# Optimization experiments

Measured on AMD Instinct MI355X. Metric: run time of the kernel, lower is better.

## Reference

```python
import jax, jax.numpy as jnp
import numpy as np

N, E, IN_FEATS, D, H, DIST_DIM, NBOUND = 10000, 160000, 128, 64, 4, 32, 31

def setup_inputs() -> dict:
    key = jax.random.key(0)
    ks = jax.random.split(key, 16)
    gain = 5.0 / 3.0  # tanh gain
    def xavier(k, shape):
        # xavier_normal over the last two dims (fan_in, fan_out) as torch does per-slice
        fan_in, fan_out = shape[-2], shape[-1]
        std = gain * np.sqrt(2.0 / (fan_in + fan_out))
        return jax.random.normal(k, shape, dtype=jnp.float32) * std
    inp = {
        'feat': jax.random.normal(ks[0], (N, IN_FEATS), dtype=jnp.float32),
        'locations': jax.random.normal(ks[1], (N, 3), dtype=jnp.float32),
        'src': jax.random.randint(ks[2], (E,), 0, N),
        'dst': jax.random.randint(ks[3], (E,), 0, N),
        'inter_ids': jax.random.randint(ks[4], (E, H), 0, N),
        'W_fc': xavier(ks[5], (IN_FEATS, H * D)),
        'embed_table': jax.random.normal(ks[6], (NBOUND + 1, DIST_DIM), dtype=jnp.float32),
        'G': xavier(ks[7], (H, DIST_DIM, D)),
        'attn_fc1': xavier(ks[8], (H, 2 * D, D)),
        'attn_fc2': xavier(ks[9], (H, 2 * D, D)),
        'attn_fc3': xavier(ks[10], (H, 2 * D, D)),
        'attn_fc': xavier(ks[11], (H, 3 * D, D)),
        'attn_out': xavier(ks[12], (H, D, 1)),
        'boundaries': jnp.linspace(0.1, 3.1, NBOUND).astype(jnp.float32),
    }
    return inp


def reference(feat, locations, W_fc, embed_table, G, attn_fc1, attn_fc2, attn_fc3,
              attn_fc, attn_out, boundaries, src, dst, inter_ids):
    n = feat.shape[0]
    h = (feat @ W_fc).reshape(n, H, D)                      # [N,H,D]
    pos = locations                                          # [N,3]
    src_pos = pos[src]                                       # [E,3]
    dst_pos = pos[dst]                                       # [E,3]
    inter_pos = pos[inter_ids]                               # [E,H,3]
    h_src = h[src]                                           # [E,H,D]
    h_dst = h[dst]                                           # [E,H,D]
    head_idx = jnp.arange(H)[None, :]
    inter_h = h[inter_ids, head_idx, :]                      # [E,H,D] per-head gather

    e_count = src.shape[0]
    dist1 = jnp.broadcast_to(jnp.linalg.norm(dst_pos - src_pos, axis=-1)[:, None], (e_count, H))
    dist2 = jnp.linalg.norm(dst_pos[:, None, :] - inter_pos, axis=-1)   # [E,H]
    dist_ = jnp.linalg.norm(src_pos[:, None, :] - inter_pos, axis=-1)   # [E,H]

    def dist_embed(dist):
        idx = jnp.searchsorted(boundaries, dist, side='left')  # torch.bucketize(right=False)
        e = embed_table[idx]                                   # [E,H,DIST_DIM]
        return jnp.einsum('ehk,hkd->ehd', e, G)                # [E,H,D]

    de1 = dist_embed(dist1)
    de2 = dist_embed(dist2)
    de_ = dist_embed(dist_)

    d1 = jnp.einsum('ehk,hkd->ehd', jnp.concatenate([h_src, de1], axis=-1), attn_fc1)
    d2 = jnp.einsum('ehk,hkd->ehd', jnp.concatenate([inter_h, de2], axis=-1), attn_fc2)
    d3 = jnp.einsum('ehk,hkd->ehd', jnp.concatenate([h_dst, de_], axis=-1), attn_fc3)

    h_c = jnp.tanh(jnp.einsum('ehk,hkd->ehd', jnp.concatenate([d1, d2, d3], axis=-1), attn_fc))
    e_score = jnp.einsum('ehd,hdo->eho', h_c, attn_out)[..., 0]        # [E,H]

    # edge softmax grouped by destination node
    m = jax.ops.segment_max(e_score, dst, num_segments=n)              # [N,H]
    ex = jnp.exp(e_score - m[dst])
    den = jax.ops.segment_sum(ex, dst, num_segments=n)                 # [N,H]
    a = ex / den[dst]                                                  # [E,H]

    ft = jax.ops.segment_sum(a[:, :, None] * h_src, dst, num_segments=n)  # [N,H,D]
    rst = jnp.mean(ft, axis=1)                                          # merge='mean' -> [N,D]
    return rst
```

## Files before the change

kernel.cpp:

```cpp
#include <hip/hip_runtime.h>
#include <hip/hip_fp16.h>
#include <math.h>

#define N_NODES 10000
#define E_EDGES 160000
#define DMODEL 64
#define H 4
#define NBOUND 31
#define SLOTS 64
#define QREC 1024

typedef _Float16 half8 __attribute__((ext_vector_type(8)));
typedef float floatx4 __attribute__((ext_vector_type(4)));

__device__ __forceinline__ void mm4(const float* __restrict__ S, int aoff,
                                    int astride, int boff, int i0, int j,
                                    int Kdim, float o[4]) {
  float a0 = 0.f, a1 = 0.f, a2 = 0.f, a3 = 0.f;
  for (int t4 = 0; t4 < (Kdim >> 2); ++t4) {
    float4 f0 = *(const float4*)&S[aoff + (i0 + 0) * astride + t4 * 4];
    float4 f1 = *(const float4*)&S[aoff + (i0 + 1) * astride + t4 * 4];
    float4 f2 = *(const float4*)&S[aoff + (i0 + 2) * astride + t4 * 4];
    float4 f3 = *(const float4*)&S[aoff + (i0 + 3) * astride + t4 * 4];
    float b0 = S[boff + (t4 * 4 + 0) * 64 + j];
    float b1 = S[boff + (t4 * 4 + 1) * 64 + j];
    float b2 = S[boff + (t4 * 4 + 2) * 64 + j];
    float b3 = S[boff + (t4 * 4 + 3) * 64 + j];
    a0 += f0.x * b0 + f0.y * b1 + f0.z * b2 + f0.w * b3;
    a1 += f1.x * b0 + f1.y * b1 + f1.z * b2 + f1.w * b3;
    a2 += f2.x * b0 + f2.y * b1 + f2.z * b2 + f2.w * b3;
    a3 += f3.x * b0 + f3.y * b1 + f3.z * b2 + f3.w * b3;
  }
  o[0] = a0; o[1] = a1; o[2] = a2; o[3] = a3;
}

__device__ __forceinline__ int didx(const float* __restrict__ bnd2, float d) {
  int g = (int)(d * 10.0f);
  g = (g < 0) ? 0 : ((g > 31) ? 31 : g);
  g += (bnd2[g + 1] < d) ? 1 : 0;
  g -= (bnd2[g] >= d) ? 1 : 0;
  return g;
}

__global__ __launch_bounds__(512) void prep_kernel(
    const float* __restrict__ fc1, const float* __restrict__ fc2,
    const float* __restrict__ fc3, const float* __restrict__ fcc,
    const float* __restrict__ Wfc, const float* __restrict__ pos,
    __half* __restrict__ bigWT, int* __restrict__ cnt,
    float4* __restrict__ pos4) {
  __shared__ __align__(16) float S[12288];
  int bi = blockIdx.x;
  int tid = threadIdx.x;
  if (bi >= 24) {
    int n = (bi - 24) * 512 + tid;
    if (n < N_NODES) {
      cnt[n] = 0;
      pos4[n] = make_float4(pos[n * 3], pos[n * 3 + 1], pos[n * 3 + 2], 0.f);
    }
    return;
  }
  int ca = bi / 12;
  int kh = bi % 12;
  int k = kh >> 2, h = kh & 3;
  const float* fck = (k == 0) ? fc1 : (k == 1) ? fc2 : fc3;
  fck += h * 128 * 64;
  const float* F = fcc + h * 192 * 64 + k * 64 * 64;
  int j = tid & 63, ig = tid >> 6;
  float o[4];
  #pragma unroll
  for (int u = 0; u < 2; ++u) {
    ((float4*)S)[u * 512 + tid] = ((const float4*)F)[u * 512 + tid];
    ((float4*)(S + 4096))[u * 512 + tid] = ((const float4*)fck)[u * 512 + tid];
  }
  __syncthreads();
  #pragma unroll
  for (int rg = 0; rg < 2; ++rg) {
    int i0 = ig * 8 + rg * 4;
    mm4(S, 4096, 64, 0, i0, j, 64, o);
    S[8192 + (i0 + 0) * 64 + j] = o[0];
    S[8192 + (i0 + 1) * 64 + j] = o[1];
    S[8192 + (i0 + 2) * 64 + j] = o[2];
    S[8192 + (i0 + 3) * 64 + j] = o[3];
  }
  __syncthreads();
  int rbase = (ca == 0) ? 0 : 64;
  #pragma unroll
  for (int u = 0; u < 2; ++u) {
    int fi = u * 512 + tid;
    int i = fi >> 4, c4 = fi & 15;
    ((float4*)(S + 4096))[fi] =
        ((const float4*)(Wfc + (rbase + i) * 256 + h * 64))[c4];
  }
  __syncthreads();
  if (k == 0) {
    #pragma unroll
    for (int u = 0; u < 8; ++u) {
      int idx = u * 512 + tid;
      int i = idx >> 6, jj = idx & 63;
      bigWT[(h * 64 + jj) * 128 + rbase + i] = __float2half(S[4096 + idx]);
    }
  }
  #pragma unroll
  for (int rg = 0; rg < 2; ++rg) {
    int i0 = ig * 8 + rg * 4;
    mm4(S, 4096, 64, 8192, i0, j, 64, o);
    int rb = ((k + 1) * 256 + h * 64 + j) * 128 + rbase;
    bigWT[rb + i0 + 0] = __float2half(o[0]);
    bigWT[rb + i0 + 1] = __float2half(o[1]);
    bigWT[rb + i0 + 2] = __float2half(o[2]);
    bigWT[rb + i0 + 3] = __float2half(o[3]);
  }
}

#define EROW 264
#define SMEM_BYTES 33792

__global__ __launch_bounds__(256) void fused_kernel(
    const float* __restrict__ feat, const __half* __restrict__ bigWT,
    __half* __restrict__ qall, const float4* __restrict__ pos4,
    const int* __restrict__ src, const int* __restrict__ dst,
    const int* __restrict__ inter, const float* __restrict__ boundaries,
    int* __restrict__ cnt, uint4* __restrict__ ebuf,
    const float* __restrict__ fc1, const float* __restrict__ fc2,
    const float* __restrict__ fc3, const float* __restrict__ fcc,
    const float* __restrict__ G, const float* __restrict__ emb,
    __half* __restrict__ U16) {
  __shared__ __align__(16) char smem[SMEM_BYTES];
  int bi = blockIdx.x;
  int tid = threadIdx.x;
  if (bi < 12) {
    float* S = (float*)smem;
    int k = bi >> 2, h = bi & 3;
    const float* fck = (k == 0) ? fc1 : (k == 1) ? fc2 : fc3;
    fck += h * 128 * 64;
    const float* F = fcc + h * 192 * 64 + k * 64 * 64;
    int j = tid & 63, ig = tid >> 6;
    #pragma unroll
    for (int u = 0; u < 4; ++u) {
      ((float4*)S)[u * 256 + tid] = ((const float4*)F)[u * 256 + tid];
      ((float4*)(S + 4096))[u * 256 + tid] =
          ((const float4*)(fck + 4096))[u * 256 + tid];
    }
    __syncthreads();
    float ob[4][4];
    #pragma unroll
    for (int rg = 0; rg < 4; ++rg)
      mm4(S, 4096, 64, 0, ig * 16 + rg * 4, j, 64, ob[rg]);
    __syncthreads();
    #pragma unroll
    for (int rg = 0; rg < 4; ++rg) {
      int i0 = ig * 16 + rg * 4;
      S[(i0 + 0) * 64 + j] = ob[rg][0];
      S[(i0 + 1) * 64 + j] = ob[rg][1];
      S[(i0 + 2) * 64 + j] = ob[rg][2];
      S[(i0 + 3) * 64 + j] = ob[rg][3];
    }
    #pragma unroll
    for (int u = 0; u < 2; ++u)
      ((float4*)(S + 4096))[u * 256 + tid] =
          ((const float4*)(G + h * 2048))[u * 256 + tid];
    ((float4*)(S + 6144))[tid] = ((const float4*)emb)[tid];
    __syncthreads();
    float og[2][4];
    #pragma unroll
    for (int rg = 0; rg < 2; ++rg)
      mm4(S, 4096, 64, 0, ig * 8 + rg * 4, j, 64, og[rg]);
    __syncthreads();
    #pragma unroll
    for (int rg = 0; rg < 2; ++rg) {
      int i0 = ig * 8 + rg * 4;
      S[(i0 + 0) * 64 + j] = og[rg][0];
      S[(i0 + 1) * 64 + j] = og[rg][1];
      S[(i0 + 2) * 64 + j] = og[rg][2];
      S[(i0 + 3) * 64 + j] = og[rg][3];
    }
    __syncthreads();
    float o[4];
    #pragma unroll
    for (int rg = 0; rg < 2; ++rg) {
      int i0 = ig * 8 + rg * 4;
      mm4(S, 6144, 32, 0, i0, j, 32, o);
      int base = k * 8192 + h * 2048;
      U16[base + (i0 + 0) * 64 + j] = __float2half(o[0]);
      U16[base + (i0 + 1) * 64 + j] = __float2half(o[1]);
      U16[base + (i0 + 2) * 64 + j] = __float2half(o[2]);
      U16[base + (i0 + 3) * 64 + j] = __float2half(o[3]);
    }
    return;
  }
  if (bi >= 640) {
    float* Sb = (float*)smem;
    if (tid < NBOUND) Sb[tid + 1] = boundaries[tid];
    if (tid == NBOUND) { Sb[0] = -INFINITY; Sb[32] = INFINITY; }
    int e = (bi - 640) * 256 + tid;
    int s = src[e], t = dst[e];
    int p = atomicAdd(&cnt[t], 1);
    int4 iv = *(const int4*)&inter[e * 4];
    int itarr[4] = {iv.x, iv.y, iv.z, iv.w};
    float4 sp = pos4[s];
    float4 tp = pos4[t];
    float4 ip0 = pos4[itarr[0]];
    float4 ip1 = pos4[itarr[1]];
    float4 ip2 = pos4[itarr[2]];
    float4 ip3 = pos4[itarr[3]];
    __syncthreads();
    float dx = tp.x - sp.x, dy = tp.y - sp.y, dz = tp.z - sp.z;
    float dist1 = sqrtf(dx * dx + dy * dy + dz * dz);
    unsigned i1 = (unsigned)didx(Sb, dist1);
    float4 ips[4] = {ip0, ip1, ip2, ip3};
    unsigned w3 = 0, q20 = 0, q_0 = 0;
    #pragma unroll
    for (int hh = 0; hh < 4; ++hh) {
      float4 ip = ips[hh];
      float ax = tp.x - ip.x, ay = tp.y - ip.y, az = tp.z - ip.z;
      float dist2 = sqrtf(ax * ax + ay * ay + az * az);
      float bx = sp.x - ip.x, by = sp.y - ip.y, bz = sp.z - ip.z;
      float dist_ = sqrtf(bx * bx + by * by + bz * bz);
      unsigned idx2 = (unsigned)didx(Sb, dist2);
      unsigned idx_ = (unsigned)didx(Sb, dist_);
      if (hh == 0) { q20 = idx2; q_0 = idx_; }
      else w3 |= (idx2 | (idx_ << 5)) << ((hh - 1) * 10);
    }
    uint4 rec;
    rec.x = (unsigned)s | ((unsigned)itarr[0] << 16);
    rec.y = (unsigned)itarr[1] | ((unsigned)itarr[2] << 16);
    rec.z = (unsigned)itarr[3] | (i1 << 16) | (q20 << 21) | (q_0 << 26);
    rec.w = w3;
    if (p < SLOTS) ebuf[t * SLOTS + p] = rec;
    return;
  }
  typedef __half EsmT[16][EROW];
  EsmT* Esm = (EsmT*)smem;
  int gi = bi - 12;
  int bx = gi % 157, by = gi / 157;
  int wv = tid >> 6, l = tid & 63;
  int m0 = bx * 64 + wv * 16;
  int n0 = by * 256;
  int lm = l & 15, lk = (l >> 4) * 8;
  int arow = m0 + lm;
  if (arow >= N_NODES) arow = N_NODES - 1;
  const float* fp = feat + arow * 128 + lk;
  const _Float16* bp = (const _Float16*)bigWT + lk;
  half8 a[4];
  #pragma unroll
  for (int kt = 0; kt < 4; ++kt) {
    float4 u0 = *(const float4*)(fp + kt * 32);
    float4 u1 = *(const float4*)(fp + kt * 32 + 4);
    half8 t;
    t[0] = (_Float16)u0.x; t[1] = (_Float16)u0.y;
    t[2] = (_Float16)u0.z; t[3] = (_Float16)u0.w;
    t[4] = (_Float16)u1.x; t[5] = (_Float16)u1.y;
    t[6] = (_Float16)u1.z; t[7] = (_Float16)u1.w;
    a[kt] = t;
  }
  #pragma unroll
  for (int nt = 0; nt < 16; ++nt) {
    floatx4 acc = (floatx4){0.f, 0.f, 0.f, 0.f};
    #pragma unroll
    for (int kt = 0; kt < 4; ++kt) {
      half8 b = *(const half8*)(bp + (n0 + nt * 16 + lm) * 128 + kt * 32);
      acc = __builtin_amdgcn_mfma_f32_16x16x32_f16(a[kt], b, acc, 0, 0, 0);
    }
    int dd = nt * 16 + lm;
    #pragma unroll
    for (int r4 = 0; r4 < 4; ++r4)
      Esm[wv][(l >> 4) * 4 + r4][dd] = __float2half(acc[r4]);
  }
  __syncthreads();
  int row = l >> 2;
  int j0 = (l & 3) * 64;
  int m = m0 + row;
  if (m < N_NODES) {
    #pragma unroll
    for (int u = 0; u < 8; ++u) {
      uint4 v = *(const uint4*)&Esm[wv][row][j0 + u * 8];
      *(uint4*)&qall[m * QREC + by * 256 + j0 + u * 8] = v;
    }
  }
}

__device__ __forceinline__ float dpp_bfly_sum16(float v) {
  int x;
  x = __builtin_amdgcn_update_dpp(0, __float_as_int(v), 0xB1, 0xf, 0xf, true);
  v += __int_as_float(x);
  x = __builtin_amdgcn_update_dpp(0, __float_as_int(v), 0x4E, 0xf, 0xf, true);
  v += __int_as_float(x);
  x = __builtin_amdgcn_update_dpp(0, __float_as_int(v), 0x141, 0xf, 0xf, true);
  v += __int_as_float(x);
  x = __builtin_amdgcn_update_dpp(0, __float_as_int(v), 0x140, 0xf, 0xf, true);
  v += __int_as_float(x);
  return v;
}

union H4u { uint2 u; __half2 h[2]; };

__device__ __forceinline__ float tanh_dot(H4u A, H4u B, H4u C, H4u X, H4u Y,
                                          H4u Z, float4 a4) {
  __half2 z0 = __hadd2(__hadd2(A.h[0], B.h[0]), __hadd2(C.h[0], X.h[0]));
  z0 = __hadd2(z0, __hadd2(Y.h[0], Z.h[0]));
  __half2 z1 = __hadd2(__hadd2(A.h[1], B.h[1]), __hadd2(C.h[1], X.h[1]));
  z1 = __hadd2(z1, __hadd2(Y.h[1], Z.h[1]));
  float2 f0 = __half22float2(z0);
  float2 f1 = __half22float2(z1);
  const float K = 2.885390082f;
  float p0 = __builtin_amdgcn_exp2f(f0.x * K);
  float p1 = __builtin_amdgcn_exp2f(f0.y * K);
  float p2 = __builtin_amdgcn_exp2f(f1.x * K);
  float p3 = __builtin_amdgcn_exp2f(f1.y * K);
  float r0 = __builtin_amdgcn_rcpf(p0 + 1.0f);
  float r1 = __builtin_amdgcn_rcpf(p1 + 1.0f);
  float r2 = __builtin_amdgcn_rcpf(p2 + 1.0f);
  float r3 = __builtin_amdgcn_rcpf(p3 + 1.0f);
  float dot = a4.x * r0;
  dot = fmaf(a4.y, r1, dot);
  dot = fmaf(a4.z, r2, dot);
  dot = fmaf(a4.w, r3, dot);
  float asum = (a4.x + a4.y) + (a4.z + a4.w);
  return fmaf(-2.0f, dot, asum);
}

__device__ __forceinline__ float4 h4_to_f4(uint2 u) {
  union { uint2 ui; __half2 h[2]; } cc;
  cc.ui = u;
  float2 a = __half22float2(cc.h[0]);
  float2 b = __half22float2(cc.h[1]);
  return make_float4(a.x, a.y, b.x, b.y);
}

__device__ __forceinline__ void dec_rec(uint4 r, int h, int* s, int* it,
                                        unsigned* i1, unsigned* q2,
                                        unsigned* q_) {
  *s = (int)(r.x & 0xffff);
  *it = (h == 0) ? (int)(r.x >> 16)
      : (h == 1) ? (int)(r.y & 0xffff)
      : (h == 2) ? (int)(r.y >> 16) : (int)(r.z & 0xffff);
  *i1 = (r.z >> 16) & 31;
  if (h == 0) {
    *q2 = (r.z >> 21) & 31;
    *q_ = (r.z >> 26) & 31;
  } else {
    unsigned f = r.w >> ((h - 1) * 10);
    *q2 = f & 31;
    *q_ = (f >> 5) & 31;
  }
}

__global__ __launch_bounds__(256) void score_agg_kernel(
    const int* __restrict__ cnt, const uint4* __restrict__ ebuf,
    const __half* __restrict__ qall, const __half* __restrict__ U16,
    const float* __restrict__ aout, float* __restrict__ out) {
  __shared__ uint4 recs[SLOTS];
  __shared__ float4 sm_num[4][64];
  __shared__ float sm_den[4][4];
  int tid = threadIdx.x;
  int w = tid >> 6, lane = tid & 63;
  int h = lane >> 4, c = lane & 15;
  int n = blockIdx.x;
  int deg = cnt[n];
  if (deg > SLOTS) deg = SLOTS;
  if (tid < deg) recs[tid] = ebuf[n * SLOTS + tid];
  H4u C;
  C.u = *(const uint2*)(qall + n * QREC + 768 + h * 64 + c * 4);
  const float4 a4 = *((const float4*)(aout + h * 64) + c);
  __syncthreads();
  float4 num = make_float4(0.f, 0.f, 0.f, 0.f);
  float den = 0.f;
  int hc4 = h * 64 + c * 4;
  for (int i = w; i < deg; i += 8) {
    int iB = i + 4;
    int vB = (iB < deg);
    uint4 rA = recs[i];
    uint4 rB = recs[vB ? iB : i];
    int sA, itA, sB, itB;
    unsigned i1A, q2A, q_A, i1B, q2B, q_B;
    dec_rec(rA, h, &sA, &itA, &i1A, &q2A, &q_A);
    dec_rec(rB, h, &sB, &itB, &i1B, &q2B, &q_B);
    H4u A0, B0, X0, Y0, Z0, A1, B1, X1, Y1, Z1;
    uint2 hr0, hr1;
    hr0 = *(const uint2*)(qall + sA * QREC + hc4);
    A0.u = *(const uint2*)(qall + sA * QREC + 256 + hc4);
    B0.u = *(const uint2*)(qall + itA * QREC + 512 + hc4);
    X0.u = *(const uint2*)(U16 + (h * 32 + (int)i1A) * 64 + c * 4);
    Y0.u = *(const uint2*)(U16 + 8192 + (h * 32 + (int)q2A) * 64 + c * 4);
    Z0.u = *(const uint2*)(U16 + 16384 + (h * 32 + (int)q_A) * 64 + c * 4);
    hr1 = *(const uint2*)(qall + sB * QREC + hc4);
    A1.u = *(const uint2*)(qall + sB * QREC + 256 + hc4);
    B1.u = *(const uint2*)(qall + itB * QREC + 512 + hc4);
    X1.u = *(const uint2*)(U16 + (h * 32 + (int)i1B) * 64 + c * 4);
    Y1.u = *(const uint2*)(U16 + 8192 + (h * 32 + (int)q2B) * 64 + c * 4);
    Z1.u = *(const uint2*)(U16 + 16384 + (h * 32 + (int)q_B) * 64 + c * 4);
    float v0 = tanh_dot(A0, B0, C, X0, Y0, Z0, a4);
    float v1 = tanh_dot(A1, B1, C, X1, Y1, Z1, a4);
    v0 = dpp_bfly_sum16(v0);
    v1 = dpp_bfly_sum16(v1);
    float ex0 = __expf(v0);
    float ex1 = vB ? __expf(v1) : 0.f;
    float4 hv0 = h4_to_f4(hr0);
    float4 hv1 = h4_to_f4(hr1);
    num.x += ex0 * hv0.x + ex1 * hv1.x;
    num.y += ex0 * hv0.y + ex1 * hv1.y;
    num.z += ex0 * hv0.z + ex1 * hv1.z;
    num.w += ex0 * hv0.w + ex1 * hv1.w;
    den += ex0 + ex1;
  }
  sm_num[w][lane] = num;
  if (c == 0) sm_den[w][h] = den;
  __syncthreads();
  if (tid < 64) {
    float4 n0 = sm_num[0][lane], n1 = sm_num[1][lane];
    float4 n2 = sm_num[2][lane], n3 = sm_num[3][lane];
    float dt = sm_den[0][h] + sm_den[1][h] + sm_den[2][h] + sm_den[3][h];
    float4 t = make_float4(0.f, 0.f, 0.f, 0.f);
    if (deg > 0) {
      float inv = 1.0f / dt;
      t.x = (n0.x + n1.x + n2.x + n3.x) * inv;
      t.y = (n0.y + n1.y + n2.y + n3.y) * inv;
      t.z = (n0.z + n1.z + n2.z + n3.z) * inv;
      t.w = (n0.w + n1.w + n2.w + n3.w) * inv;
    }
    t.x += __shfl_xor(t.x, 16); t.y += __shfl_xor(t.y, 16);
    t.z += __shfl_xor(t.z, 16); t.w += __shfl_xor(t.w, 16);
    t.x += __shfl_xor(t.x, 32); t.y += __shfl_xor(t.y, 32);
    t.z += __shfl_xor(t.z, 32); t.w += __shfl_xor(t.w, 32);
    if (h == 0) {
      t.x *= 0.25f; t.y *= 0.25f; t.z *= 0.25f; t.w *= 0.25f;
      *(float4*)&out[n * 64 + c * 4] = t;
    }
  }
}

extern "C" void kernel_launch(void* const* d_in, const int* in_sizes, int n_in,
                              void* d_out, int out_size, void* d_ws,
                              size_t ws_size, hipStream_t stream) {
  const float* feat = (const float*)d_in[0];
  const float* loc = (const float*)d_in[1];
  const int* src = (const int*)d_in[2];
  const int* dst = (const int*)d_in[3];
  const int* inter = (const int*)d_in[4];
  const float* Wfc = (const float*)d_in[5];
  const float* emb = (const float*)d_in[6];
  const float* G = (const float*)d_in[7];
  const float* fc1 = (const float*)d_in[8];
  const float* fc2 = (const float*)d_in[9];
  const float* fc3 = (const float*)d_in[10];
  const float* fcc = (const float*)d_in[11];
  const float* aout = (const float*)d_in[12];
  const float* bnd = (const float*)d_in[13];
  float* out = (float*)d_out;

  __half* qall = (__half*)d_ws;
  __half* bigWT = qall + N_NODES * QREC;
  __half* U16 = bigWT + 1024 * 128;
  uint4* ebuf = (uint4*)(U16 + 3 * H * 2048);
  int* cnt = (int*)(ebuf + N_NODES * SLOTS);
  float4* pos4 = (float4*)(cnt + N_NODES);

  prep_kernel<<<44, 512, 0, stream>>>(fc1, fc2, fc3, fcc, Wfc, loc, bigWT,
                                      cnt, pos4);
  fused_kernel<<<1265, 256, 0, stream>>>(feat, bigWT, qall, pos4, src, dst,
                                         inter, bnd, cnt, ebuf, fc1, fc2, fc3,
                                         fcc, G, emb, U16);
  score_agg_kernel<<<N_NODES, 256, 0, stream>>>(cnt, ebuf, qall, U16, aout,
                                                out);
}
```

Baseline: 173.8 us.

## Interleave h and src-projection rows in qall and retile projection GEMM

The projection GEMM is retiled so each block computes 16 rows by 512 columns, with one wave per 128-column slice, instead of 64 rows by 256 columns. The first half's output is interleaved so each node's h and A-projection values for a given head/chunk sit in one 16-byte segment. The aggregation kernel then fetches both with a single uint4 gather per edge instead of two uint2 gathers, and it reads edge records straight from global memory instead of staging them in shared memory behind a barrier. This trades fewer, wider random gathers and one less sync for more GEMM blocks and repeated record loads per wave.

```diff
diff --git a/kernel.cpp b/kernel.cpp
--- a/kernel.cpp
+++ b/kernel.cpp
@@ -112,8 +112,8 @@
   }
 }
 
-#define EROW 264
-#define SMEM_BYTES 33792
+#define EROW2 520
+#define SMEM_BYTES 32768
 
 __global__ __launch_bounds__(256) void fused_kernel(
     const float* __restrict__ feat, const __half* __restrict__ bigWT,
@@ -188,11 +188,11 @@
     }
     return;
   }
-  if (bi >= 640) {
+  if (bi >= 1262) {
     float* Sb = (float*)smem;
     if (tid < NBOUND) Sb[tid + 1] = boundaries[tid];
     if (tid == NBOUND) { Sb[0] = -INFINITY; Sb[32] = INFINITY; }
-    int e = (bi - 640) * 256 + tid;
+    int e = (bi - 1262) * 256 + tid;
     int s = src[e], t = dst[e];
     int p = atomicAdd(&cnt[t], 1);
     int4 iv = *(const int4*)&inter[e * 4];
@@ -229,18 +229,15 @@
     if (p < SLOTS) ebuf[t * SLOTS + p] = rec;
     return;
   }
-  typedef __half EsmT[16][EROW];
-  EsmT* Esm = (EsmT*)smem;
+  typedef __half Erow[EROW2];
+  Erow* Esm = (Erow*)smem;
   int gi = bi - 12;
-  int bx = gi % 157, by = gi / 157;
+  int bx = gi % 625, half = gi / 625;
   int wv = tid >> 6, l = tid & 63;
-  int m0 = bx * 64 + wv * 16;
-  int n0 = by * 256;
+  int m0 = bx * 16;
   int lm = l & 15, lk = (l >> 4) * 8;
-  int arow = m0 + lm;
-  if (arow >= N_NODES) arow = N_NODES - 1;
-  const float* fp = feat + arow * 128 + lk;
-  const _Float16* bp = (const _Float16*)bigWT + lk;
+  const float* fp = feat + (m0 + lm) * 128 + lk;
+  const _Float16* bp = (const _Float16*)bigWT + lk + (half * 512 + wv * 128) * 128;
   half8 a[4];
   #pragma unroll
   for (int kt = 0; kt < 4; ++kt) {
@@ -254,27 +251,36 @@
     a[kt] = t;
   }
   #pragma unroll
-  for (int nt = 0; nt < 16; ++nt) {
+  for (int nt = 0; nt < 8; ++nt) {
     floatx4 acc = (floatx4){0.f, 0.f, 0.f, 0.f};
     #pragma unroll
     for (int kt = 0; kt < 4; ++kt) {
-      half8 b = *(const half8*)(bp + (n0 + nt * 16 + lm) * 128 + kt * 32);
+      half8 b = *(const half8*)(bp + (nt * 16 + lm) * 128 + kt * 32);
       acc = __builtin_amdgcn_mfma_f32_16x16x32_f16(a[kt], b, acc, 0, 0, 0);
     }
-    int dd = nt * 16 + lm;
+    int dd = wv * 128 + nt * 16 + lm;
     #pragma unroll
     for (int r4 = 0; r4 < 4; ++r4)
-      Esm[wv][(l >> 4) * 4 + r4][dd] = __float2half(acc[r4]);
+      Esm[(l >> 4) * 4 + r4][dd] = __float2half(acc[r4]);
   }
   __syncthreads();
-  int row = l >> 2;
-  int j0 = (l & 3) * 64;
-  int m = m0 + row;
-  if (m < N_NODES) {
-    #pragma unroll
-    for (int u = 0; u < 8; ++u) {
-      uint4 v = *(const uint4*)&Esm[wv][row][j0 + u * 8];
-      *(uint4*)&qall[m * QREC + by * 256 + j0 + u * 8] = v;
+  int r = tid >> 4, q = tid & 15;
+  int m = m0 + r;
+  if (half == 0) {
+    #pragma unroll
+    for (int u = 0; u < 4; ++u) {
+      int g = q + u * 16;
+      uint2 hp = *(const uint2*)&Esm[r][g * 4];
+      uint2 qp = *(const uint2*)&Esm[r][256 + g * 4];
+      uint4 v = make_uint4(hp.x, hp.y, qp.x, qp.y);
+      *(uint4*)&qall[m * QREC + g * 8] = v;
+    }
+  } else {
+    #pragma unroll
+    for (int u = 0; u < 4; ++u) {
+      int g2 = q + u * 16;
+      uint4 v = *(const uint4*)&Esm[r][g2 * 8];
+      *(uint4*)&qall[m * QREC + 512 + g2 * 8] = v;
     }
   }
 }
@@ -293,6 +299,7 @@
 }
 
 union H4u { uint2 u; __half2 h[2]; };
+union H8u { uint4 u4; __half2 h2[4]; };
 
 __device__ __forceinline__ float tanh_dot(H4u A, H4u B, H4u C, H4u X, H4u Y,
                                           H4u Z, float4 a4) {
@@ -319,14 +326,6 @@
   return fmaf(-2.0f, dot, asum);
 }
 
-__device__ __forceinline__ float4 h4_to_f4(uint2 u) {
-  union { uint2 ui; __half2 h[2]; } cc;
-  cc.ui = u;
-  float2 a = __half22float2(cc.h[0]);
-  float2 b = __half22float2(cc.h[1]);
-  return make_float4(a.x, a.y, b.x, b.y);
-}
-
 __device__ __forceinline__ void dec_rec(uint4 r, int h, int* s, int* it,
                                         unsigned* i1, unsigned* q2,
                                         unsigned* q_) {
@@ -349,7 +348,6 @@
     const int* __restrict__ cnt, const uint4* __restrict__ ebuf,
     const __half* __restrict__ qall, const __half* __restrict__ U16,
     const float* __restrict__ aout, float* __restrict__ out) {
-  __shared__ uint4 recs[SLOTS];
   __shared__ float4 sm_num[4][64];
   __shared__ float sm_den[4][4];
   int tid = threadIdx.x;
@@ -358,49 +356,52 @@
   int n = blockIdx.x;
   int deg = cnt[n];
   if (deg > SLOTS) deg = SLOTS;
-  if (tid < deg) recs[tid] = ebuf[n * SLOTS + tid];
   H4u C;
   C.u = *(const uint2*)(qall + n * QREC + 768 + h * 64 + c * 4);
   const float4 a4 = *((const float4*)(aout + h * 64) + c);
-  __syncthreads();
   float4 num = make_float4(0.f, 0.f, 0.f, 0.f);
   float den = 0.f;
   int hc4 = h * 64 + c * 4;
+  int g8 = hc4 * 2;
+  const uint4* eb = ebuf + n * SLOTS;
   for (int i = w; i < deg; i += 8) {
     int iB = i + 4;
     int vB = (iB < deg);
-    uint4 rA = recs[i];
-    uint4 rB = recs[vB ? iB : i];
+    uint4 rA = eb[i];
+    uint4 rB = eb[vB ? iB : i];
     int sA, itA, sB, itB;
     unsigned i1A, q2A, q_A, i1B, q2B, q_B;
     dec_rec(rA, h, &sA, &itA, &i1A, &q2A, &q_A);
     dec_rec(rB, h, &sB, &itB, &i1B, &q2B, &q_B);
-    H4u A0, B0, X0, Y0, Z0, A1, B1, X1, Y1, Z1;
-    uint2 hr0, hr1;
-    hr0 = *(const uint2*)(qall + sA * QREC + hc4);
-    A0.u = *(const uint2*)(qall + sA * QREC + 256 + hc4);
+    H8u AH0, AH1;
+    H4u B0, X0, Y0, Z0, B1, X1, Y1, Z1;
+    AH0.u4 = *(const uint4*)(qall + sA * QREC + g8);
     B0.u = *(const uint2*)(qall + itA * QREC + 512 + hc4);
     X0.u = *(const uint2*)(U16 + (h * 32 + (int)i1A) * 64 + c * 4);
     Y0.u = *(const uint2*)(U16 + 8192 + (h * 32 + (int)q2A) * 64 + c * 4);
     Z0.u = *(const uint2*)(U16 + 16384 + (h * 32 + (int)q_A) * 64 + c * 4);
-    hr1 = *(const uint2*)(qall + sB * QREC + hc4);
-    A1.u = *(const uint2*)(qall + sB * QREC + 256 + hc4);
+    AH1.u4 = *(const uint4*)(qall + sB * QREC + g8);
     B1.u = *(const uint2*)(qall + itB * QREC + 512 + hc4);
     X1.u = *(const uint2*)(U16 + (h * 32 + (int)i1B) * 64 + c * 4);
     Y1.u = *(const uint2*)(U16 + 8192 + (h * 32 + (int)q2B) * 64 + c * 4);
     Z1.u = *(const uint2*)(U16 + 16384 + (h * 32 + (int)q_B) * 64 + c * 4);
+    H4u A0, A1;
+    A0.h[0] = AH0.h2[2]; A0.h[1] = AH0.h2[3];
+    A1.h[0] = AH1.h2[2]; A1.h[1] = AH1.h2[3];
     float v0 = tanh_dot(A0, B0, C, X0, Y0, Z0, a4);
     float v1 = tanh_dot(A1, B1, C, X1, Y1, Z1, a4);
     v0 = dpp_bfly_sum16(v0);
     v1 = dpp_bfly_sum16(v1);
     float ex0 = __expf(v0);
     float ex1 = vB ? __expf(v1) : 0.f;
-    float4 hv0 = h4_to_f4(hr0);
-    float4 hv1 = h4_to_f4(hr1);
-    num.x += ex0 * hv0.x + ex1 * hv1.x;
-    num.y += ex0 * hv0.y + ex1 * hv1.y;
-    num.z += ex0 * hv0.z + ex1 * hv1.z;
-    num.w += ex0 * hv0.w + ex1 * hv1.w;
+    float2 h00 = __half22float2(AH0.h2[0]);
+    float2 h01 = __half22float2(AH0.h2[1]);
+    float2 h10 = __half22float2(AH1.h2[0]);
+    float2 h11 = __half22float2(AH1.h2[1]);
+    num.x += ex0 * h00.x + ex1 * h10.x;
+    num.y += ex0 * h00.y + ex1 * h10.y;
+    num.z += ex0 * h01.x + ex1 * h11.x;
+    num.w += ex0 * h01.y + ex1 * h11.y;
     den += ex0 + ex1;
   }
   sm_num[w][lane] = num;
@@ -457,7 +458,7 @@
 
   prep_kernel<<<44, 512, 0, stream>>>(fc1, fc2, fc3, fcc, Wfc, loc, bigWT,
                                       cnt, pos4);
-  fused_kernel<<<1265, 256, 0, stream>>>(feat, bigWT, qall, pos4, src, dst,
+  fused_kernel<<<1887, 256, 0, stream>>>(feat, bigWT, qall, pos4, src, dst,
                                          inter, bnd, cnt, ebuf, fc1, fc2, fc3,
                                          fcc, G, emb, U16);
   score_agg_kernel<<<N_NODES, 256, 0, stream>>>(cnt, ebuf, qall, U16, aout,
```

Measured after the change: 172.8 us. No clear change (-0.6%).
